# Optimization experiments

Hardware: AMD Instinct MI355X
Metric: run time of the kernel (lower is better)

The kernel has to match this reference:

```python
import jax, jax.numpy as jnp
import numpy as np
from jax import lax

C, S, G = 128, 4, 8
CG = C // G   # 16 channels per group branch
CS = C // S   # 32 channels per SPC slab
EPS = 1e-5
REGION, HALF = 5, 2


def conv2d(x, w, b, pad):
    y = lax.conv_general_dilated(x, w, (1, 1), [(pad, pad), (pad, pad)],
                                 dimension_numbers=('NCHW', 'OIHW', 'NCHW'))
    return y + b[None, :, None, None]


def setup_inputs() -> dict:
    key = jax.random.key(0)
    ks = jax.random.split(key, 16)
    B, H, W = 16, 152, 272
    sc = 0.05
    inp = {
        'x': jax.random.normal(ks[0], (B, C, H, W), jnp.float32),
        'detections': jax.random.randint(ks[1], (B, S, 4), 0, 148, dtype=jnp.int32),
        'w1': jax.random.normal(ks[2], (CG, CG, 1, 1), jnp.float32) * sc,
        'b1': jax.random.normal(ks[3], (CG,), jnp.float32) * sc,
        'w3': jax.random.normal(ks[4], (CG, CG, 3, 3), jnp.float32) * sc,
        'b3': jax.random.normal(ks[5], (CG,), jnp.float32) * sc,
        'gn_w': jnp.ones((CG,), jnp.float32),
        'gn_b': jnp.zeros((CG,), jnp.float32),
    }
    for i in range(S):
        k = 2 * (i + 1) + 1
        inp[f'cw{i}'] = jax.random.normal(ks[6 + 2 * i], (CS, CS, k, k), jnp.float32) * sc
        inp[f'cb{i}'] = jax.random.normal(ks[7 + 2 * i], (CS,), jnp.float32) * sc
    return inp


def reference(x, detections, w1, b1, w3, b3, gn_w, gn_b,
              cw0, cb0, cw1, cb1, cw2, cb2, cw3, cb3):
    b, c, h, w = x.shape
    gx = x.reshape(b * G, CG, h, w)
    # coordinate attention: pool over W and H
    x_h = gx.mean(axis=3, keepdims=True)                           # [bG,CG,h,1]
    x_w = gx.mean(axis=2, keepdims=True).transpose(0, 1, 3, 2)      # [bG,CG,w,1]
    hw = conv2d(jnp.concatenate([x_h, x_w], axis=2), w1, b1, 0)
    xh, xw = hw[:, :, :h], hw[:, :, h:]
    pre = gx * jax.nn.sigmoid(xh) * jax.nn.sigmoid(xw.transpose(0, 1, 3, 2))
    # GroupNorm(num_groups == num_channels) == per-channel instance norm
    mu = pre.mean(axis=(2, 3), keepdims=True)
    var = pre.var(axis=(2, 3), keepdims=True)
    x1 = (pre - mu) / jnp.sqrt(var + EPS) * gn_w[None, :, None, None] + gn_b[None, :, None, None]
    x2 = conv2d(gx, w3, b3, 1)
    x11 = jax.nn.softmax(x1.mean(axis=(2, 3)).reshape(b * G, 1, CG), axis=-1)
    x12 = x2.reshape(b * G, CG, h * w)
    x21 = jax.nn.softmax(x2.mean(axis=(2, 3)).reshape(b * G, 1, CG), axis=-1)
    x22 = x1.reshape(b * G, CG, h * w)
    weights = (jnp.matmul(x11, x12) + jnp.matmul(x21, x22)).reshape(b * G, 1, h, w)
    spc = (gx * jax.nn.sigmoid(weights)).reshape(b, S, CS, h, w)

    conv_ws = [cw0, cw1, cw2, cw3]
    conv_bs = [cb0, cb1, cb2, cb3]
    gather = jax.vmap(lambda s, y0, x0: lax.dynamic_slice(s, (0, y0, x0), (CS, REGION, REGION)))
    scatter = jax.vmap(lambda s, r, y0, x0: lax.dynamic_update_slice(s, r, (0, y0, x0)))
    for idx in range(S):
        cx = detections[:, idx, 0]
        cy = detections[:, idx, 1]
        valid = (cy >= HALF) & (cy < h - HALF) & (cx >= HALF) & (cx < w - HALF)
        ys = jnp.clip(cy - HALF, 0, h - REGION)
        xs = jnp.clip(cx - HALF, 0, w - REGION)
        slab = spc[:, idx]                                          # [b,CS,h,w]
        regions = gather(slab, ys, xs)                              # [b,CS,5,5]
        regions = jnp.where(valid[:, None, None, None], regions, 0.0)
        conv_out = conv2d(regions, conv_ws[idx], conv_bs[idx], idx + 1)  # stays 5x5
        new_slab = scatter(slab, conv_out, ys, xs)
        slab = jnp.where(valid[:, None, None, None], new_slab, slab)
        spc = spc.at[:, idx].set(slab)

    sig = jax.nn.sigmoid(spc)
    out = x + (spc * sig).reshape(b, c, h, w)
    # channel shuffle with groups=G
    out = out.reshape(b, G, c // G, h, w).transpose(0, 2, 1, 3, 4).reshape(b, c, h, w)
    return out
```

## Files before the change

### kernel.cpp

```cpp
#include <hip/hip_runtime.h>
#include <math.h>

#define H_ 152
#define W_ 272
#define HW_ 41344
#define W4_ 68
#define HW4_ 10336
#define B_ 16
#define G_ 8
#define CG_ 16
#define NG_ 128
#define PC_ 2048
#define S_ 4
#define EPSV 1e-5f
#define NTILE_ 162

__device__ __forceinline__ float sigf(float v){ return 1.0f/(1.0f+__expf(-v)); }

__global__ void k_stats1(const float* __restrict__ x, float* __restrict__ xh,
                         float* __restrict__ xw){
  int plane = blockIdx.x;
  const float* xp = x + (size_t)plane*HW_;
  int tid = threadIdx.x, wv = tid>>6, lane = tid&63;
  float ca0[4] = {0,0,0,0};
  float ca1[4] = {0,0,0,0};
  for (int h = wv; h < H_; h += 4){
    const float4* row = (const float4*)(xp + h*W_);
    float4 v0 = row[lane];
    float rs = v0.x+v0.y+v0.z+v0.w;
    ca0[0]+=v0.x; ca0[1]+=v0.y; ca0[2]+=v0.z; ca0[3]+=v0.w;
    if (lane < 4){
      float4 v1 = row[64+lane];
      rs += v1.x+v1.y+v1.z+v1.w;
      ca1[0]+=v1.x; ca1[1]+=v1.y; ca1[2]+=v1.z; ca1[3]+=v1.w;
    }
    #pragma unroll
    for (int off=32; off>0; off>>=1) rs += __shfl_down(rs, off, 64);
    if (lane==0) xh[plane*H_ + h] = rs * (1.0f/W_);
  }
  __shared__ float cs[4][W_];
  #pragma unroll
  for (int j=0;j<4;++j) cs[wv][lane*4+j] = ca0[j];
  if (lane<4){
    #pragma unroll
    for (int j=0;j<4;++j) cs[wv][256+lane*4+j] = ca1[j];
  }
  __syncthreads();
  for (int w=tid; w<W_; w+=256)
    xw[plane*W_ + w] = (cs[0][w]+cs[1][w]+cs[2][w]+cs[3][w]) * (1.0f/H_);
}

__global__ void k_prep(const float* __restrict__ x,
                       const float* __restrict__ xh, const float* __restrict__ xw,
                       const float* __restrict__ w1, const float* __restrict__ b1,
                       const float* __restrict__ w3, const float* __restrict__ b3,
                       const float* __restrict__ gnb,
                       float* __restrict__ sh, float* __restrict__ sw,
                       float* __restrict__ x21, float* __restrict__ wsum,
                       float* __restrict__ bsum){
  int bg = blockIdx.x; int tid = threadIdx.x;
  __shared__ float xhl[CG_][H_];
  __shared__ float xwl[CG_][W_];
  __shared__ float w1l[CG_*CG_];
  __shared__ float b1l[CG_];
  __shared__ float Tk[CG_], R0[CG_], RL[CG_], C0[CG_], CL[CG_];
  __shared__ float crn[CG_][4];
  __shared__ float mx2[CG_], x11l[CG_];
  for (int i=tid;i<CG_*CG_;i+=256) w1l[i]=w1[i];
  if (tid < CG_) b1l[tid]=b1[tid];
  for (int i=tid;i<CG_*H_;i+=256){ int c=i/H_, h=i%H_; xhl[c][h]=xh[(bg*CG_+c)*H_+h]; }
  for (int i=tid;i<CG_*W_;i+=256){ int c=i/W_, w=i%W_; xwl[c][w]=xw[(bg*CG_+c)*W_+w]; }
  __syncthreads();
  for (int i=tid;i<CG_*H_;i+=256){
    int c=i/H_, h=i%H_;
    float a=b1l[c];
    #pragma unroll
    for (int k=0;k<CG_;++k) a += w1l[c*CG_+k]*xhl[k][h];
    sh[(bg*CG_+c)*H_+h] = sigf(a);
  }
  for (int i=tid;i<CG_*W_;i+=256){
    int c=i/W_, w=i%W_;
    float a=b1l[c];
    #pragma unroll
    for (int k=0;k<CG_;++k) a += w1l[c*CG_+k]*xwl[k][w];
    sw[(bg*CG_+c)*W_+w] = sigf(a);
  }
  if (tid < CG_){
    int k=tid;
    float t=0;
    for (int h=0;h<H_;++h) t += xhl[k][h];
    Tk[k] = t * W_;
    R0[k] = xhl[k][0]*W_; RL[k]=xhl[k][H_-1]*W_;
    C0[k] = xwl[k][0]*H_; CL[k]=xwl[k][W_-1]*H_;
    const float* xp = x + (size_t)(bg*CG_+k)*HW_;
    crn[k][0]=xp[0]; crn[k][1]=xp[W_-1];
    crn[k][2]=xp[(size_t)(H_-1)*W_]; crn[k][3]=xp[(size_t)(H_-1)*W_+W_-1];
  }
  __syncthreads();
  if (tid < CG_){
    int c=tid;
    float acc=0;
    for (int k=0;k<CG_;++k){
      #pragma unroll
      for (int ky=0;ky<3;++ky){ int dy=ky-1;
        #pragma unroll
        for (int kx=0;kx<3;++kx){ int dx=kx-1;
          float s = Tk[k];
          if (dy==1) s -= R0[k]; else if (dy==-1) s -= RL[k];
          if (dx==1) s -= C0[k]; else if (dx==-1) s -= CL[k];
          if (dy==1 && dx==1) s += crn[k][0];
          else if (dy==1 && dx==-1) s += crn[k][1];
          else if (dy==-1 && dx==1) s += crn[k][2];
          else if (dy==-1 && dx==-1) s += crn[k][3];
          acc += w3[((c*CG_+k)*3+ky)*3+kx]*s;
        }
      }
    }
    mx2[c] = b3[c] + acc*(1.0f/HW_);
  }
  __syncthreads();
  if (tid==0){
    float m=mx2[0]; for (int c=1;c<CG_;++c) m=fmaxf(m,mx2[c]);
    float ssum=0.f; float e[CG_];
    for (int c=0;c<CG_;++c){ e[c]=__expf(mx2[c]-m); ssum+=e[c]; }
    for (int c=0;c<CG_;++c) x21[bg*CG_+c]=e[c]/ssum;
    float m2=gnb[0]; for (int c=1;c<CG_;++c) m2=fmaxf(m2,gnb[c]);
    float s2=0.f; float e2[CG_];
    for (int c=0;c<CG_;++c){ e2[c]=__expf(gnb[c]-m2); s2+=e2[c]; }
    float bs=0.f;
    for (int c=0;c<CG_;++c){ x11l[c]=e2[c]/s2; bs += (e2[c]/s2)*b3[c]; }
    bsum[bg]=bs;
  }
  __syncthreads();
  for (int i=tid;i<CG_*9;i+=256){
    int k=i/9, r=i%9; int ky=r/3, kx=r%3;
    float a=0;
    for (int c=0;c<CG_;++c) a += x11l[c]*w3[((c*CG_+k)*3+ky)*3+kx];
    wsum[bg*CG_*9 + i] = a;
  }
}

__global__ void k_stats2(const float* __restrict__ x, const float* __restrict__ sh,
                         const float* __restrict__ sw, float* __restrict__ mu,
                         float* __restrict__ rstd){
  int plane = blockIdx.x; int tid=threadIdx.x;
  __shared__ float shl[H_]; __shared__ float swl[W_];
  for (int i=tid;i<H_;i+=256) shl[i]=sh[plane*H_+i];
  for (int i=tid;i<W_;i+=256) swl[i]=sw[plane*W_+i];
  __syncthreads();
  const float4* xp = (const float4*)(x + (size_t)plane*HW_);
  float s=0, s2=0;
  for (int i4=tid; i4<HW_/4; i4+=256){
    int p = i4*4; int h=p/W_, w=p%W_;
    float4 v = xp[i4];
    float shv = shl[h];
    float p0 = v.x*shv*swl[w], p1=v.y*shv*swl[w+1];
    float p2 = v.z*shv*swl[w+2], p3=v.w*shv*swl[w+3];
    s  += p0+p1+p2+p3;
    s2 += p0*p0+p1*p1+p2*p2+p3*p3;
  }
  __shared__ float rs[4], rs2[4];
  #pragma unroll
  for (int off=32; off>0; off>>=1){ s += __shfl_down(s,off,64); s2 += __shfl_down(s2,off,64); }
  int wv=tid>>6, lane=tid&63;
  if (lane==0){ rs[wv]=s; rs2[wv]=s2; }
  __syncthreads();
  if (tid==0){
    float S1=rs[0]+rs[1]+rs[2]+rs[3], S2=rs2[0]+rs2[1]+rs2[2]+rs2[3];
    float m = S1*(1.0f/HW_);
    float v = S2*(1.0f/HW_)-m*m;
    mu[plane]=m; rstd[plane]=rsqrtf(v+EPSV);
  }
}

__global__ void k_coef(const float* __restrict__ x21, const float* __restrict__ gnw,
                       const float* __restrict__ gnb, const float* __restrict__ mu,
                       const float* __restrict__ rstd, const float* __restrict__ bsum,
                       float* __restrict__ alpha, float* __restrict__ wconst){
  int bg = blockIdx.x; int tid=threadIdx.x;
  float contrib = 0.f;
  if (tid < CG_){
    int plane = bg*CG_+tid;
    float t21 = x21[plane];
    alpha[plane] = t21*gnw[tid]*rstd[plane];
    contrib = t21*(gnb[tid] - mu[plane]*rstd[plane]*gnw[tid]);
  }
  #pragma unroll
  for (int off=8; off>0; off>>=1) contrib += __shfl_down(contrib, off, 64);
  if (tid==0) wconst[bg] = bsum[bg] + contrib;
}

__global__ void k_weights(const float* __restrict__ x, const float* __restrict__ sh,
                          const float* __restrict__ sw, const float* __restrict__ alpha,
                          const float* __restrict__ wsum, const float* __restrict__ wconst,
                          float* __restrict__ wout, float* __restrict__ out){
  int wgid = blockIdx.x + blockIdx.y*gridDim.x;
  int swz  = (wgid & 7)*(NTILE_*NG_/8) + (wgid >> 3);
  int bg   = swz / NTILE_;
  int tile = swz % NTILE_;
  int tid = threadIdx.x;
  int ty = tid>>6, lane = tid&63;
  int i4 = tile*64 + lane;
  bool ok = (i4 < HW4_);
  int i4c = ok ? i4 : (HW4_-1);
  int w4 = i4c % W4_, h = i4c / W4_;
  int p  = i4c*4;
  bool hm=(h>0), hp=(h<H_-1), wm=(w4>0), wp=(w4<W4_-1);
  const float4 z4 = {0.f,0.f,0.f,0.f};

  __shared__ float wsl[CG_*9];
  __shared__ float all[CG_];
  __shared__ float shl[CG_][2];
  int h0 = (tile*64) / W4_;
  if (tid < CG_*9) wsl[tid] = wsum[bg*CG_*9 + tid];
  else if (tid < CG_*9 + CG_) all[tid - CG_*9] = alpha[bg*CG_ + (tid - CG_*9)];
  else if (tid < CG_*9 + CG_ + 2*CG_){
    int t = tid - CG_*9 - CG_;
    int c = t>>1, r = t&1;
    int hh = h0 + r; if (hh > H_-1) hh = H_-1;
    shl[c][r] = sh[(bg*CG_+c)*H_ + hh];
  }
  __syncthreads();

  float4 acc = z4;
  const float* xp0 = x + (size_t)(bg*CG_ + ty*4)*HW_;
  float4 v0 = *(const float4*)(xp0 + p);
  float4 vm = hm ? *(const float4*)(xp0 + p - W_) : z4;
  float4 vp = hp ? *(const float4*)(xp0 + p + W_) : z4;
  float4 swv = *(const float4*)(&sw[(bg*CG_ + ty*4)*W_ + w4*4]);

  #pragma unroll 1
  for (int j=0;j<4;++j){
    int c = ty*4 + j;
    const float* xp = x + (size_t)(bg*CG_+c)*HW_;
    float4 n0=z4, nm=z4, np=z4, nsw=z4;
    if (j<3){
      const float* xn = xp + HW_;
      n0 = *(const float4*)(xn + p);
      nm = hm ? *(const float4*)(xn + p - W_) : z4;
      np = hp ? *(const float4*)(xn + p + W_) : z4;
      nsw = *(const float4*)(&sw[(bg*CG_+c+1)*W_ + w4*4]);
    }
    float lm = __shfl_up(vm.w, 1, 64);
    float l0 = __shfl_up(v0.w, 1, 64);
    float lp = __shfl_up(vp.w, 1, 64);
    float rm = __shfl_down(vm.x, 1, 64);
    float r0 = __shfl_down(v0.x, 1, 64);
    float rp = __shfl_down(vp.x, 1, 64);
    if (!wm){ lm=0.f; l0=0.f; lp=0.f; }
    if (!wp){ rm=0.f; r0=0.f; rp=0.f; }
    if (lane==0 || lane==63){
      bool L = (lane==0);
      bool en = L ? wm : wp;
      int q = L ? (p-1) : (p+4);
      float em = (en&&hm) ? xp[q-W_] : 0.f;
      float e0 = en        ? xp[q]    : 0.f;
      float ep = (en&&hp) ? xp[q+W_] : 0.f;
      if (L){ lm=em; l0=e0; lp=ep; } else { rm=em; r0=e0; rp=ep; }
    }
    float a = all[c] * shl[c][h - h0];
    const float* wr = wsl + c*9;
    float w0=wr[0], w1v=wr[1], w2=wr[2], w3v=wr[3], w4v=wr[4];
    float w5=wr[5], w6=wr[6], w7=wr[7], w8=wr[8];
    acc.x += a*swv.x*v0.x + w0*lm   + w1v*vm.x + w2*vm.y
           + w3v*l0       + w4v*v0.x + w5*v0.y
           + w6*lp        + w7*vp.x + w8*vp.y;
    acc.y += a*swv.y*v0.y + w0*vm.x + w1v*vm.y + w2*vm.z
           + w3v*v0.x     + w4v*v0.y + w5*v0.z
           + w6*vp.x      + w7*vp.y + w8*vp.z;
    acc.z += a*swv.z*v0.z + w0*vm.y + w1v*vm.z + w2*vm.w
           + w3v*v0.y     + w4v*v0.z + w5*v0.w
           + w6*vp.y      + w7*vp.z + w8*vp.w;
    acc.w += a*swv.w*v0.w + w0*vm.z + w1v*vm.w + w2*rm
           + w3v*v0.z     + w4v*v0.w + w5*r0
           + w6*vp.z      + w7*vp.w + w8*rp;
    v0 = n0; vm = nm; vp = np; swv = nsw;
  }

  __shared__ float4 part[4][64];
  part[ty][lane] = acc;
  __syncthreads();

  float4 p0v = part[0][lane], p1v = part[1][lane];
  float4 p2v = part[2][lane], p3v = part[3][lane];
  float wc = wconst[bg];
  float4 tot;
  tot.x = p0v.x+p1v.x+p2v.x+p3v.x + wc;
  tot.y = p0v.y+p1v.y+p2v.y+p3v.y + wc;
  tot.z = p0v.z+p1v.z+p2v.z+p3v.z + wc;
  tot.w = p0v.w+p1v.w+p2v.w+p3v.w + wc;

  if (ty==0 && ok) *(float4*)(wout + (size_t)bg*HW_ + p) = tot;

  float4 gv;
  gv.x = sigf(tot.x); gv.y = sigf(tot.y); gv.z = sigf(tot.z); gv.w = sigf(tot.w);
  int b = bg>>3, g = bg&7;
  if (ok){
    #pragma unroll 1
    for (int j=0;j<4;++j){
      int c = ty*4 + j;
      const float* xp = x + (size_t)(bg*CG_+c)*HW_;
      float4 cv = *(const float4*)(xp + p);
      float* ob = out + (size_t)(b*128 + c*8 + g)*HW_ + p;
      float4 o; float s;
      s = cv.x*gv.x; o.x = cv.x + s*sigf(s);
      s = cv.y*gv.y; o.y = cv.y + s*sigf(s);
      s = cv.z*gv.z; o.z = cv.z + s*sigf(s);
      s = cv.w*gv.w; o.w = cv.w + s*sigf(s);
      *(float4*)ob = o;
    }
  }
}

__global__ void k_fix(const float* __restrict__ x, const float* __restrict__ wout,
                      const int* __restrict__ det,
                      const float* __restrict__ cw0, const float* __restrict__ cb0,
                      const float* __restrict__ cw1, const float* __restrict__ cb1,
                      const float* __restrict__ cw2, const float* __restrict__ cb2,
                      const float* __restrict__ cw3, const float* __restrict__ cb3,
                      float* __restrict__ out){
  int blk = blockIdx.x;
  int co = blk & 31;
  int bi = blk >> 5;
  int b = bi>>2, idx = bi&3;
  int cx = det[(b*S_+idx)*4+0], cy = det[(b*S_+idx)*4+1];
  if (!(cy>=2 && cy<H_-2 && cx>=2 && cx<W_-2)) return;
  int ys = cy-2, xs = cx-2;
  int k = 2*idx+3, pad = idx+1, kk = k*k;
  const float* cw = idx==0?cw0: idx==1?cw1: idx==2?cw2:cw3;
  const float* cb = idx==0?cb0: idx==1?cb1: idx==2?cb2:cb3;
  __shared__ float reg[32*25];
  __shared__ float wl[32*81];
  int tid = threadIdx.x;
  for (int t=tid;t<800;t+=64){
    int ci=t/25, r=t%25, ry=r/5, rx=r%5;
    int g = idx*2 + (ci>>4), cg = ci&15;
    int bg = b*G_+g; int plane = bg*CG_+cg;
    int p = (ys+ry)*W_ + xs+rx;
    reg[t] = x[(size_t)plane*HW_+p]*sigf(wout[(size_t)bg*HW_+p]);
  }
  for (int t=tid;t<32*kk;t+=64) wl[t] = cw[co*32*kk + t];
  __syncthreads();
  int pix = (tid<25)?tid:(tid-25);
  int half = (tid<25)?0:1;
  float acc = 0.f;
  if (tid < 50){
    int oy = pix/5, ox = pix%5;
    for (int ci=half*16; ci<half*16+16; ++ci){
      const float* wr = wl + ci*kk;
      const float* rr = reg + ci*25;
      #pragma unroll
      for (int iy=0; iy<5; ++iy){
        int ky = iy-oy+pad;
        if ((unsigned)ky >= (unsigned)k) continue;
        #pragma unroll
        for (int ix=0; ix<5; ++ix){
          int kx = ix-ox+pad;
          if ((unsigned)kx >= (unsigned)k) continue;
          acc += wr[ky*k+kx]*rr[iy*5+ix];
        }
      }
    }
  }
  float other = __shfl(acc, tid+25, 64);
  if (tid < 25){
    float tot = cb[co] + acc + other;
    int oy = pix/5, ox = pix%5;
    int g = idx*2 + (co>>4), cg = co&15;
    int bg = b*G_+g; int plane = bg*CG_+cg;
    int p = (ys+oy)*W_ + xs+ox;
    float xv = x[(size_t)plane*HW_+p];
    out[(size_t)(b*128 + cg*8 + g)*HW_+p] = xv + tot*sigf(tot);
  }
}

extern "C" void kernel_launch(void* const* d_in, const int* in_sizes, int n_in,
                              void* d_out, int out_size, void* d_ws, size_t ws_size,
                              hipStream_t stream){
  const float* x   = (const float*)d_in[0];
  const int*   det = (const int*)d_in[1];
  const float* w1  = (const float*)d_in[2];
  const float* b1  = (const float*)d_in[3];
  const float* w3  = (const float*)d_in[4];
  const float* b3  = (const float*)d_in[5];
  const float* gnw = (const float*)d_in[6];
  const float* gnb = (const float*)d_in[7];
  const float* cw0 = (const float*)d_in[8];  const float* cb0 = (const float*)d_in[9];
  const float* cw1 = (const float*)d_in[10]; const float* cb1 = (const float*)d_in[11];
  const float* cw2 = (const float*)d_in[12]; const float* cb2 = (const float*)d_in[13];
  const float* cw3 = (const float*)d_in[14]; const float* cb3 = (const float*)d_in[15];

  float* ws = (float*)d_ws;
  float* xh    = ws;
  float* xw    = xh + PC_*H_;
  float* sh    = xw + PC_*W_;
  float* sw    = sh + PC_*H_;
  float* mu    = sw + PC_*W_;
  float* rstd  = mu + PC_;
  float* x21   = rstd + PC_;
  float* alpha = x21 + PC_;
  float* wsum  = alpha + PC_;
  float* bsum  = wsum + NG_*144;
  float* wconst= bsum + NG_;
  float* wout  = wconst + NG_;
  float* outp  = (float*)d_out;

  k_stats1<<<PC_,256,0,stream>>>(x, xh, xw);
  k_prep<<<NG_,256,0,stream>>>(x, xh, xw, w1,b1,w3,b3,gnb, sh,sw,x21,wsum,bsum);
  k_stats2<<<PC_,256,0,stream>>>(x, sh, sw, mu, rstd);
  k_coef<<<NG_,64,0,stream>>>(x21,gnw,gnb,mu,rstd,bsum,alpha,wconst);
  dim3 gw(NTILE_, NG_);
  k_weights<<<gw,256,0,stream>>>(x, sh, sw, alpha, wsum, wconst, wout, outp);
  k_fix<<<B_*S_*32,64,0,stream>>>(x, wout, det, cw0,cb0,cw1,cb1,cw2,cb2,cw3,cb3, outp);
}
```

Before: 396.1 us.

## Use nontemporal stores, prefetch halo edges, and reverse stats2 plane order

Output and wout writes in the main fused kernel become nontemporal stores, so write-once data does not pollute the cache. The edge-lane halo loads for the next channel are now prefetched alongside the main float4 loads instead of being loaded on demand inside the loop. k_stats2 walks planes in reverse, so the planes most recently touched by the previous kernel are read first and are more likely to hit in cache. Risks include extra registers for the prefetched values and nontemporal stores hurting k_fix if it rereads those outputs.

```diff
diff --git a/kernel.cpp b/kernel.cpp
--- a/kernel.cpp
+++ b/kernel.cpp
@@ -14,6 +14,13 @@
 #define S_ 4
 #define EPSV 1e-5f
 #define NTILE_ 162
+
+typedef float nfloat4 __attribute__((ext_vector_type(4)));
+
+__device__ __forceinline__ void nt_store4(float* p, float4 v){
+  nfloat4 t; t.x=v.x; t.y=v.y; t.z=v.z; t.w=v.w;
+  __builtin_nontemporal_store(t, (nfloat4*)p);
+}
 
 __device__ __forceinline__ float sigf(float v){ return 1.0f/(1.0f+__expf(-v)); }
 
@@ -143,7 +150,7 @@
 __global__ void k_stats2(const float* __restrict__ x, const float* __restrict__ sh,
                          const float* __restrict__ sw, float* __restrict__ mu,
                          float* __restrict__ rstd){
-  int plane = blockIdx.x; int tid=threadIdx.x;
+  int plane = (PC_-1) - blockIdx.x; int tid=threadIdx.x;
   __shared__ float shl[H_]; __shared__ float swl[W_];
   for (int i=tid;i<H_;i+=256) shl[i]=sh[plane*H_+i];
   for (int i=tid;i<W_;i+=256) swl[i]=sw[plane*W_+i];
@@ -222,24 +229,41 @@
   }
   __syncthreads();
 
+  bool eact = (lane==0 || lane==63);
+  bool eL   = (lane==0);
+  bool een  = eact && (eL ? wm : wp);
+  int  eq   = eL ? (p-1) : (p+4);
+
   float4 acc = z4;
-  const float* xp0 = x + (size_t)(bg*CG_ + ty*4)*HW_;
+  int cbase = ty*4;
+  const float* xp0 = x + (size_t)(bg*CG_ + cbase)*HW_;
   float4 v0 = *(const float4*)(xp0 + p);
   float4 vm = hm ? *(const float4*)(xp0 + p - W_) : z4;
   float4 vp = hp ? *(const float4*)(xp0 + p + W_) : z4;
-  float4 swv = *(const float4*)(&sw[(bg*CG_ + ty*4)*W_ + w4*4]);
+  float4 swv = *(const float4*)(&sw[(bg*CG_+cbase)*W_ + w4*4]);
+  float em=0.f, e0=0.f, ep=0.f;
+  if (een){
+    e0 = xp0[eq];
+    if (hm) em = xp0[eq-W_];
+    if (hp) ep = xp0[eq+W_];
+  }
 
   #pragma unroll 1
   for (int j=0;j<4;++j){
-    int c = ty*4 + j;
-    const float* xp = x + (size_t)(bg*CG_+c)*HW_;
+    int c = cbase + j;
     float4 n0=z4, nm=z4, np=z4, nsw=z4;
+    float fm=0.f, f0=0.f, fp=0.f;
     if (j<3){
-      const float* xn = xp + HW_;
+      const float* xn = x + (size_t)(bg*CG_+c+1)*HW_;
       n0 = *(const float4*)(xn + p);
       nm = hm ? *(const float4*)(xn + p - W_) : z4;
       np = hp ? *(const float4*)(xn + p + W_) : z4;
       nsw = *(const float4*)(&sw[(bg*CG_+c+1)*W_ + w4*4]);
+      if (een){
+        f0 = xn[eq];
+        if (hm) fm = xn[eq-W_];
+        if (hp) fp = xn[eq+W_];
+      }
     }
     float lm = __shfl_up(vm.w, 1, 64);
     float l0 = __shfl_up(v0.w, 1, 64);
@@ -249,15 +273,8 @@
     float rp = __shfl_down(vp.x, 1, 64);
     if (!wm){ lm=0.f; l0=0.f; lp=0.f; }
     if (!wp){ rm=0.f; r0=0.f; rp=0.f; }
-    if (lane==0 || lane==63){
-      bool L = (lane==0);
-      bool en = L ? wm : wp;
-      int q = L ? (p-1) : (p+4);
-      float em = (en&&hm) ? xp[q-W_] : 0.f;
-      float e0 = en        ? xp[q]    : 0.f;
-      float ep = (en&&hp) ? xp[q+W_] : 0.f;
-      if (L){ lm=em; l0=e0; lp=ep; } else { rm=em; r0=e0; rp=ep; }
-    }
+    if (lane==0){ lm=em; l0=e0; lp=ep; }
+    else if (lane==63){ rm=em; r0=e0; rp=ep; }
     float a = all[c] * shl[c][h - h0];
     const float* wr = wsl + c*9;
     float w0=wr[0], w1v=wr[1], w2=wr[2], w3v=wr[3], w4v=wr[4];
@@ -275,6 +292,7 @@
            + w3v*v0.z     + w4v*v0.w + w5*r0
            + w6*vp.z      + w7*vp.w + w8*rp;
     v0 = n0; vm = nm; vp = np; swv = nsw;
+    em = fm; e0 = f0; ep = fp;
   }
 
   __shared__ float4 part[4][64];
@@ -290,7 +308,8 @@
   tot.z = p0v.z+p1v.z+p2v.z+p3v.z + wc;
   tot.w = p0v.w+p1v.w+p2v.w+p3v.w + wc;
 
-  if (ty==0 && ok) *(float4*)(wout + (size_t)bg*HW_ + p) = tot;
+  if (ty==0 && ok)
+    nt_store4(wout + (size_t)bg*HW_ + p, tot);
 
   float4 gv;
   gv.x = sigf(tot.x); gv.y = sigf(tot.y); gv.z = sigf(tot.z); gv.w = sigf(tot.w);
@@ -307,7 +326,7 @@
       s = cv.y*gv.y; o.y = cv.y + s*sigf(s);
       s = cv.z*gv.z; o.z = cv.z + s*sigf(s);
       s = cv.w*gv.w; o.w = cv.w + s*sigf(s);
-      *(float4*)ob = o;
+      nt_store4(ob, o);
     }
   }
 }
```

Result: faster. 366.3 us (-7.5%).
